# Kernel optimization log

Measured on AMD Instinct MI355X. Metric: run time of the kernel, lower is better.

## Reference

```python
import jax, jax.numpy as jnp
import numpy as np

H = 300          # node_hidden_dim (GINE output dim)
D = 2 * H        # set2set in_channels = 600
STEPS = 2        # num_step_set2_set


def _lstm_cell(x, h, c, W_ih, W_hh, b_ih, b_hh):
    # PyTorch LSTM gate order: i, f, g, o
    gates = x @ W_ih.T + h @ W_hh.T + b_ih + b_hh
    i, f, g, o = jnp.split(gates, 4, axis=-1)
    c = jax.nn.sigmoid(f) * c + jax.nn.sigmoid(i) * jnp.tanh(g)
    h = jax.nn.sigmoid(o) * jnp.tanh(c)
    return h, c


def _set2set(x, batch, num_graphs, W_ih, W_hh, b_ih, b_hh):
    # torch_geometric Set2Set with processing_steps=STEPS, 1-layer LSTM
    B = num_graphs
    q_star = jnp.zeros((B, 2 * D), x.dtype)
    h = jnp.zeros((B, D), x.dtype)
    c = jnp.zeros((B, D), x.dtype)
    for _ in range(STEPS):
        h, c = _lstm_cell(q_star, h, c, W_ih, W_hh, b_ih, b_hh)
        q = h                                   # [B, D]
        e = jnp.sum(x * q[batch], axis=-1)      # [N]
        emax = jax.ops.segment_max(e, batch, num_segments=B)
        a = jnp.exp(e - emax[batch])
        asum = jax.ops.segment_sum(a, batch, num_segments=B)
        a = a / (asum[batch] + 1e-16)           # segment softmax
        r = jax.ops.segment_sum(a[:, None] * x, batch, num_segments=B)
        q_star = jnp.concatenate([q, r], axis=-1)   # [B, 2D]
    return q_star


def _l2norm(x):
    return x / jnp.maximum(jnp.linalg.norm(x, axis=1, keepdims=True), 1e-12)


def setup_inputs() -> dict:
    key = jax.random.key(0)
    ks = jax.random.split(key, 8)
    Nu, Nv, B = 8192, 8192, 256
    solute_x = jax.random.normal(ks[0], (Nu, H), jnp.float32)
    solvent_x = jax.random.normal(ks[1], (Nv, H), jnp.float32)
    solute_batch = jnp.sort(jax.random.randint(ks[2], (Nu,), 0, B)).astype(jnp.int32)
    solvent_batch = jnp.sort(jax.random.randint(ks[3], (Nv,), 0, B)).astype(jnp.int32)
    lstm_W_ih = jax.random.normal(ks[4], (4 * D, 2 * D), jnp.float32) * 0.02
    lstm_W_hh = jax.random.normal(ks[5], (4 * D, D), jnp.float32) * 0.02
    lstm_b_ih = jnp.zeros((4 * D,), jnp.float32)
    lstm_b_hh = jnp.zeros((4 * D,), jnp.float32)
    pred_W = jax.random.normal(ks[6], (1, 8 * H), jnp.float32) * 0.02
    pred_b = jnp.zeros((1,), jnp.float32)
    return {
        "solute_x": solute_x, "solvent_x": solvent_x,
        "solute_batch": solute_batch, "solvent_batch": solvent_batch,
        "num_graphs": B,
        "lstm_W_ih": lstm_W_ih, "lstm_W_hh": lstm_W_hh,
        "lstm_b_ih": lstm_b_ih, "lstm_b_hh": lstm_b_hh,
        "pred_W": pred_W, "pred_b": pred_b,
    }


def reference(solute_x, solvent_x, solute_batch, solvent_batch, num_graphs,
              lstm_W_ih, lstm_W_hh, lstm_b_ih, lstm_b_hh, pred_W, pred_b):
    # F.normalize(dim=1)
    su = _l2norm(solute_x)    # [Nu, H]
    sv = _l2norm(solvent_x)   # [Nv, H]
    # len_map = solute_len.T @ solvent_len == same-pair membership mask
    mask = (solute_batch[:, None] == solvent_batch[None, :]).astype(su.dtype)
    interaction_map = (su @ sv.T) * mask          # [Nu, Nv]
    ret_interaction_map = interaction_map
    solvent_prime = interaction_map.T @ su        # [Nv, H]
    solute_prime = interaction_map @ sv           # [Nu, H]
    su2 = jnp.concatenate([su, solute_prime], axis=1)    # [Nu, 2H]
    sv2 = jnp.concatenate([sv, solvent_prime], axis=1)   # [Nv, 2H]
    su_s2s = _set2set(su2, solute_batch, num_graphs, lstm_W_ih, lstm_W_hh, lstm_b_ih, lstm_b_hh)
    sv_s2s = _set2set(sv2, solvent_batch, num_graphs, lstm_W_ih, lstm_W_hh, lstm_b_ih, lstm_b_hh)
    final = jnp.concatenate([su_s2s, sv_s2s], axis=1)    # [B, 8H]
    predictions = final @ pred_W.T + pred_b              # [B, 1]
    return predictions, ret_interaction_map
```

## Files before the change

kernel.cpp:

```cpp
#include <hip/hip_runtime.h>
#include <math.h>

#define HDIM 300
#define DDIM 600
#define NGR  256

typedef float vf4 __attribute__((ext_vector_type(4)));

__device__ __forceinline__ float wred_sum(float v){
  #pragma unroll
  for(int o=32;o;o>>=1) v += __shfl_xor(v,o,64);
  return v;
}
__device__ __forceinline__ float wred_max(float v){
  #pragma unroll
  for(int o=32;o;o>>=1) v = fmaxf(v,__shfl_xor(v,o,64));
  return v;
}
__device__ __forceinline__ float sigm(float x){ return 1.f/(1.f+expf(-x)); }

__global__ __launch_bounds__(256) void k_norm(const float* __restrict__ xu,
    const float* __restrict__ xv, float* __restrict__ su, float* __restrict__ sv,
    int Nu, int Nv){
  int wid = (blockIdx.x * 256 + threadIdx.x) >> 6;
  int lane = threadIdx.x & 63;
  if (wid >= Nu + Nv) return;
  const float* src; float* dst;
  if (wid < Nu){ src = xu + (size_t)wid*HDIM; dst = su + (size_t)wid*HDIM; }
  else         { src = xv + (size_t)(wid-Nu)*HDIM; dst = sv + (size_t)(wid-Nu)*HDIM; }
  float v[5]; float s = 0.f;
  #pragma unroll
  for(int c=0;c<5;c++){ int k = lane + 64*c; float x = (k<HDIM)? src[k] : 0.f; v[c]=x; s += x*x; }
  s = wred_sum(s);
  float inv = 1.f / fmaxf(sqrtf(s), 1e-12f);
  #pragma unroll
  for(int c=0;c<5;c++){ int k = lane + 64*c; if (k<HDIM) dst[k] = v[c]*inv; }
}

__global__ __launch_bounds__(640) void k_off_h1(const int* __restrict__ ub,
    const int* __restrict__ vb, int Nu, int Nv, int* __restrict__ uoff,
    int* __restrict__ voff, const float* __restrict__ b_ih,
    const float* __restrict__ b_hh, float* __restrict__ h1, float* __restrict__ c1){
  int t = threadIdx.x;
  if (t < NGR){
    int lo=0, hi=Nu;
    while(lo<hi){ int mid=(lo+hi)>>1; if (ub[mid] < t) lo=mid+1; else hi=mid; }
    uoff[t]=lo; if (t==0) uoff[NGR]=Nu;
  } else if (t < 2*NGR){
    int g=t-NGR; int lo=0, hi=Nv;
    while(lo<hi){ int mid=(lo+hi)>>1; if (vb[mid] < g) lo=mid+1; else hi=mid; }
    voff[g]=lo; if (g==0) voff[NGR]=Nv;
  }
  if (t < DDIM){
    float gi = b_ih[t]        + b_hh[t];
    float gg = b_ih[1200+t]   + b_hh[1200+t];
    float go = b_ih[1800+t]   + b_hh[1800+t];
    float c  = sigm(gi)*tanhf(gg);
    c1[t]=c; h1[t]=sigm(go)*tanhf(c);
  }
}

template<bool WRITE_MAP>
__global__ __launch_bounds__(256) void k_prime(const float* __restrict__ xa,
    const float* __restrict__ xb, const int* __restrict__ mybatch,
    const int* __restrict__ ooff, float* __restrict__ prime,
    float* __restrict__ eout, const float* __restrict__ h1,
    float* __restrict__ mapbase, int Nother){
  int i = blockIdx.x;
  int tid = threadIdx.x, lane = tid & 63, w = tid >> 6;
  __shared__ float xrow[HDIM];
  __shared__ float qv[2*HDIM];
  __shared__ float prl[4*304];
  __shared__ float red[4];
  const float* rowp = xa + (size_t)i*HDIM;
  for (int t=tid; t<HDIM;   t+=256) xrow[t] = rowp[t];
  for (int t=tid; t<2*HDIM; t+=256) qv[t]   = h1[t];
  int g = mybatch[i];
  int js = ooff[g], je = ooff[g+1];
  __syncthreads();
  if (WRITE_MAP){
    float* mrow = mapbase + (size_t)i*Nother;
    const vf4 z4 = {0.f,0.f,0.f,0.f};
    int nf4 = Nother >> 2;
    for (int q4=tid; q4<nf4; q4+=256){
      int j0 = q4*4;
      if (j0+4 <= js || j0 >= je){
        __builtin_nontemporal_store(z4, (vf4*)(mrow + j0));
      } else {
        #pragma unroll
        for(int u=0;u<4;u++){ int j=j0+u; if (j<js || j>=je) mrow[j]=0.f; }
      }
    }
  }
  float pr[5];
  #pragma unroll
  for(int c=0;c<5;c++) pr[c]=0.f;
  for (int j = js + w; j < je; j += 4){
    const float* orow = xb + (size_t)j*HDIM;
    float xv[5]; float d = 0.f;
    #pragma unroll
    for(int c=0;c<5;c++){
      int k = lane + 64*c; float x=0.f, a=0.f;
      if (k<HDIM){ x = orow[k]; a = xrow[k]; }
      xv[c]=x; d += a*x;
    }
    d = wred_sum(d);
    if (WRITE_MAP && lane==0) mapbase[(size_t)i*Nother + j] = d;
    #pragma unroll
    for(int c=0;c<5;c++) pr[c] += d * xv[c];
  }
  #pragma unroll
  for(int c=0;c<5;c++){ int k = lane + 64*c; if (k<HDIM) prl[w*304 + k] = pr[c]; }
  __syncthreads();
  float ep = 0.f;
  for (int t=tid; t<HDIM; t+=256){
    float s = prl[t] + prl[304+t] + prl[608+t] + prl[912+t];
    prime[(size_t)i*HDIM + t] = s;
    ep += xrow[t]*qv[t] + s*qv[HDIM+t];
  }
  ep = wred_sum(ep);
  if (lane==0) red[w] = ep;
  __syncthreads();
  if (tid==0) eout[i] = red[0]+red[1]+red[2]+red[3];
}

__global__ __launch_bounds__(256) void k_r1(const float* __restrict__ su,
    const float* __restrict__ sv, const float* __restrict__ spr,
    const float* __restrict__ svp, const float* __restrict__ e1u,
    const float* __restrict__ e1v, const int* __restrict__ uoff,
    const int* __restrict__ voff, float* __restrict__ r1){
  int bs = blockIdx.x; int set = bs >> 8; int g = bs & 255;
  const float* x  = set? sv  : su;
  const float* pr = set? svp : spr;
  const float* e  = set? e1v : e1u;
  const int* off  = set? voff: uoff;
  int tid = threadIdx.x, lane = tid & 63, w = tid >> 6;
  __shared__ float al[2048]; __shared__ float red[4]; __shared__ float shv;
  int ns = off[g], ne = off[g+1]; int n = ne - ns;
  float m = -INFINITY;
  for (int t=ns+tid; t<ne; t+=256) m = fmaxf(m, e[t]);
  m = wred_max(m);
  if (lane==0) red[w]=m;
  __syncthreads();
  if (tid==0) shv = fmaxf(fmaxf(red[0],red[1]),fmaxf(red[2],red[3]));
  __syncthreads();
  float emax = shv;
  float s = 0.f;
  for (int t=tid; t<n; t+=256){ float a = expf(e[ns+t]-emax); if (t<2048) al[t]=a; s += a; }
  s = wred_sum(s);
  __syncthreads();
  if (lane==0) red[w]=s;
  __syncthreads();
  if (tid==0) shv = red[0]+red[1]+red[2]+red[3];
  __syncthreads();
  float inv = 1.f/(shv + 1e-16f);
  float acc[3] = {0.f,0.f,0.f};
  for (int nn=0; nn<n; nn++){
    float a = (nn<2048)? al[nn] : expf(e[ns+nn]-emax);
    const float* xr = x  + (size_t)(ns+nn)*HDIM;
    const float* pp = pr + (size_t)(ns+nn)*HDIM;
    #pragma unroll
    for(int u=0;u<3;u++){ int c = tid + u*256; if (c<DDIM){
        float xv = (c<HDIM)? xr[c] : pp[c-HDIM]; acc[u] += a*xv; } }
  }
  #pragma unroll
  for(int u=0;u<3;u++){ int c = tid + u*256; if (c<DDIM) r1[(size_t)bs*DDIM + c] = acc[u]*inv; }
}

__global__ __launch_bounds__(256) void k_gbase(const float* __restrict__ h1,
    const float* __restrict__ Wih, const float* __restrict__ Whh,
    const float* __restrict__ b_ih, const float* __restrict__ b_hh,
    float* __restrict__ gbase){
  int n = blockIdx.x*4 + (threadIdx.x >> 6); int lane = threadIdx.x & 63;
  if (n >= 2400) return;
  const float* wi = Wih + (size_t)n*1200;
  const float* wh = Whh + (size_t)n*600;
  float s = 0.f;
  for (int k=lane; k<DDIM; k+=64) s += h1[k]*(wi[k] + wh[k]);
  s = wred_sum(s);
  if (lane==0) gbase[n] = s + b_ih[n] + b_hh[n];
}

__global__ __launch_bounds__(256) void k_gemm(const float* __restrict__ r1,
    const float* __restrict__ Wih, float* __restrict__ g2){
  __shared__ __align__(16) float Al[16*64];
  __shared__ __align__(16) float Bl[16*64];
  int tid = threadIdx.x;
  int n0 = blockIdx.x*64, gs0 = blockIdx.y*64;
  int tx = tid & 15, ty = tid >> 4;
  int lk = tid & 15, lr = tid >> 4;
  float acc[4][4] = {};
  for (int kt=0; kt<600; kt+=16){
    int k = kt + lk;
    #pragma unroll
    for (int u=0; u<4; u++){
      int gl = lr + u*16;
      Al[lk*64 + gl] = (k<600)? r1[(size_t)(gs0+gl)*DDIM + k] : 0.f;
      int n = n0 + gl;
      Bl[lk*64 + gl] = (k<600 && n<2400)? Wih[(size_t)n*1200 + 600 + k] : 0.f;
    }
    __syncthreads();
    #pragma unroll
    for (int kk=0; kk<16; kk++){
      float4 av = *(const float4*)&Al[kk*64 + ty*4];
      float4 bv = *(const float4*)&Bl[kk*64 + tx*4];
      float a[4]={av.x,av.y,av.z,av.w}, b[4]={bv.x,bv.y,bv.z,bv.w};
      #pragma unroll
      for(int mm=0;mm<4;mm++)
        #pragma unroll
        for(int nn=0;nn<4;nn++) acc[mm][nn] += a[mm]*b[nn];
    }
    __syncthreads();
  }
  #pragma unroll
  for (int mm=0; mm<4; mm++){
    int gs = gs0 + ty*4 + mm;
    int n  = n0 + tx*4;
    if (n+4 <= 2400){
      float4 o = make_float4(acc[mm][0],acc[mm][1],acc[mm][2],acc[mm][3]);
      *(float4*)&g2[(size_t)gs*2400 + n] = o;
    } else {
      #pragma unroll
      for(int nn=0;nn<4;nn++) if (n+nn<2400) g2[(size_t)gs*2400 + n+nn] = acc[mm][nn];
    }
  }
}

__global__ __launch_bounds__(256) void k_lstm2(const float* __restrict__ g2,
    const float* __restrict__ gbase, const float* __restrict__ c1,
    float* __restrict__ h2){
  int idx = blockIdx.x*256 + threadIdx.x;
  if (idx >= 512*DDIM) return;
  int gs = idx / DDIM, d = idx - gs*DDIM;
  const float* gg = g2 + (size_t)gs*2400;
  float gi = gg[d]        + gbase[d];
  float gf = gg[600+d]    + gbase[600+d];
  float gG = gg[1200+d]   + gbase[1200+d];
  float go = gg[1800+d]   + gbase[1800+d];
  float c  = sigm(gf)*c1[d] + sigm(gi)*tanhf(gG);
  h2[idx] = sigm(go)*tanhf(c);
}

__global__ __launch_bounds__(256) void k_r2(const float* __restrict__ su,
    const float* __restrict__ sv, const float* __restrict__ spr,
    const float* __restrict__ svp, const int* __restrict__ uoff,
    const int* __restrict__ voff, const float* __restrict__ h2,
    const float* __restrict__ pW, float* __restrict__ e2u,
    float* __restrict__ e2v, float* __restrict__ ppart){
  int bs = blockIdx.x; int set = bs >> 8; int g = bs & 255;
  const float* x  = set? sv  : su;
  const float* pr = set? svp : spr;
  const int* off  = set? voff: uoff;
  float* e2       = set? e2v : e2u;
  int tid = threadIdx.x, lane = tid & 63, w = tid >> 6;
  __shared__ float q[DDIM]; __shared__ float al[2048];
  __shared__ float red[4]; __shared__ float shv;
  for (int t=tid; t<DDIM; t+=256) q[t] = h2[(size_t)bs*DDIM + t];
  int ns = off[g], ne = off[g+1]; int n = ne - ns;
  __syncthreads();
  for (int node = ns + w; node < ne; node += 4){
    const float* xr = x  + (size_t)node*HDIM;
    const float* pp = pr + (size_t)node*HDIM;
    float d = 0.f;
    #pragma unroll
    for(int c=0;c<10;c++){ int k = lane + 64*c; if (k<DDIM){
        float xv = (k<HDIM)? xr[k] : pp[k-HDIM]; d += xv*q[k]; } }
    d = wred_sum(d);
    if (lane==0) e2[node] = d;
  }
  __syncthreads();
  float m = -INFINITY;
  for (int t=ns+tid; t<ne; t+=256) m = fmaxf(m, e2[t]);
  m = wred_max(m);
  if (lane==0) red[w]=m;
  __syncthreads();
  if (tid==0) shv = fmaxf(fmaxf(red[0],red[1]),fmaxf(red[2],red[3]));
  __syncthreads();
  float emax = shv;
  float s = 0.f;
  for (int t=tid; t<n; t+=256){ float a = expf(e2[ns+t]-emax); if (t<2048) al[t]=a; s += a; }
  s = wred_sum(s);
  __syncthreads();
  if (lane==0) red[w]=s;
  __syncthreads();
  if (tid==0) shv = red[0]+red[1]+red[2]+red[3];
  __syncthreads();
  float inv = 1.f/(shv + 1e-16f);
  float acc[3] = {0.f,0.f,0.f};
  for (int nn=0; nn<n; nn++){
    float a = (nn<2048)? al[nn] : expf(e2[ns+nn]-emax);
    const float* xr = x  + (size_t)(ns+nn)*HDIM;
    const float* pp = pr + (size_t)(ns+nn)*HDIM;
    #pragma unroll
    for(int u=0;u<3;u++){ int c = tid + u*256; if (c<DDIM){
        float xv = (c<HDIM)? xr[c] : pp[c-HDIM]; acc[u] += a*xv; } }
  }
  int hoff = set? 1200 : 0;
  float p = 0.f;
  #pragma unroll
  for(int u=0;u<3;u++){ int c = tid + u*256; if (c<DDIM) p += (acc[u]*inv)*pW[hoff+600+c]; }
  for (int t=tid; t<DDIM; t+=256) p += q[t]*pW[hoff+t];
  p = wred_sum(p);
  __syncthreads();
  if (lane==0) red[w] = p;
  __syncthreads();
  if (tid==0) ppart[bs] = red[0]+red[1]+red[2]+red[3];
}

__global__ __launch_bounds__(256) void k_pred(const float* __restrict__ ppart,
    const float* __restrict__ pred_b, float* __restrict__ out){
  int g = threadIdx.x;
  out[g] = ppart[g] + ppart[NGR+g] + pred_b[0];
}

extern "C" void kernel_launch(void* const* d_in, const int* in_sizes, int n_in,
                              void* d_out, int out_size, void* d_ws, size_t ws_size,
                              hipStream_t stream) {
  const float* solute_x  = (const float*)d_in[0];
  const float* solvent_x = (const float*)d_in[1];
  const int*   ub        = (const int*)d_in[2];
  const int*   vb        = (const int*)d_in[3];
  const float* Wih  = (const float*)d_in[5];
  const float* Whh  = (const float*)d_in[6];
  const float* b_ih = (const float*)d_in[7];
  const float* b_hh = (const float*)d_in[8];
  const float* pW   = (const float*)d_in[9];
  const float* pb   = (const float*)d_in[10];

  int Nu = in_sizes[0] / HDIM;
  int Nv = in_sizes[1] / HDIM;

  float* out = (float*)d_out;
  int predn = out_size - Nu*Nv;
  float* mapbase = out + predn;

  float* ws = (float*)d_ws;
  float* su    = ws;
  float* sv    = su    + (size_t)Nu*HDIM;
  float* spr   = sv    + (size_t)Nv*HDIM;
  float* svp   = spr   + (size_t)Nu*HDIM;
  float* e1u   = svp   + (size_t)Nv*HDIM;
  float* e1v   = e1u   + Nu;
  float* h1    = e1v   + Nv;
  float* c1    = h1    + DDIM;
  float* r1    = c1    + DDIM;
  float* gbase = r1    + 512*DDIM;
  float* g2    = gbase + 2400;
  float* h2    = g2    + (size_t)512*2400;
  float* ppart = h2    + 512*DDIM;
  int*   uoff  = (int*)(ppart + 512);
  int*   voff  = uoff + 257;

  k_norm<<<dim3((Nu+Nv)/4), dim3(256), 0, stream>>>(solute_x, solvent_x, su, sv, Nu, Nv);
  k_off_h1<<<dim3(1), dim3(640), 0, stream>>>(ub, vb, Nu, Nv, uoff, voff, b_ih, b_hh, h1, c1);
  k_prime<true ><<<dim3(Nu), dim3(256), 0, stream>>>(su, sv, ub, voff, spr, e1u, h1, mapbase, Nv);
  k_prime<false><<<dim3(Nv), dim3(256), 0, stream>>>(sv, su, vb, uoff, svp, e1v, h1, nullptr, Nv);
  k_r1<<<dim3(512), dim3(256), 0, stream>>>(su, sv, spr, svp, e1u, e1v, uoff, voff, r1);
  k_gbase<<<dim3(600), dim3(256), 0, stream>>>(h1, Wih, Whh, b_ih, b_hh, gbase);
  k_gemm<<<dim3(38, 8), dim3(256), 0, stream>>>(r1, Wih, g2);
  k_lstm2<<<dim3((512*DDIM + 255)/256), dim3(256), 0, stream>>>(g2, gbase, c1, h2);
  k_r2<<<dim3(512), dim3(256), 0, stream>>>(su, sv, spr, svp, uoff, voff, h2, pW, e1u, e1v, ppart);
  k_pred<<<dim3(1), dim3(NGR), 0, stream>>>(ppart, pb, out);
}
```

Before: 590.9 us.

## Fuse kernels, vectorize row loads, and fold LSTM gating into gate GEMM

Merges ten launches into five. Normalization is combined with offset and h1 setup, the two prime passes become one grid, and the r1 and gbase kernels share a launch. The gate GEMM is re-tiled so each block holds all four gates for 16 hidden units, which lets it apply the LSTM cell in its epilogue and drops the g2 round trip through memory. Row loads move to float4 vectors, and the final prediction is accumulated with atomics into an output pre-seeded with the bias. The goal is to cut launch overhead and intermediate global traffic, at the cost of atomic ordering nondeterminism and heterogeneous block roles.

```diff
diff --git a/kernel.cpp b/kernel.cpp
--- a/kernel.cpp
+++ b/kernel.cpp
@@ -19,58 +19,70 @@
 }
 __device__ __forceinline__ float sigm(float x){ return 1.f/(1.f+expf(-x)); }
 
-__global__ __launch_bounds__(256) void k_norm(const float* __restrict__ xu,
+__global__ __launch_bounds__(256) void k_norm_off(const float* __restrict__ xu,
     const float* __restrict__ xv, float* __restrict__ su, float* __restrict__ sv,
-    int Nu, int Nv){
-  int wid = (blockIdx.x * 256 + threadIdx.x) >> 6;
+    int Nu, int Nv, const int* __restrict__ ub, const int* __restrict__ vb,
+    int* __restrict__ uoff, int* __restrict__ voff,
+    const float* __restrict__ b_ih, const float* __restrict__ b_hh,
+    float* __restrict__ h1, float* __restrict__ c1,
+    const float* __restrict__ pb, float* __restrict__ outp){
+  if (blockIdx.x == gridDim.x - 1){
+    int t = threadIdx.x;
+    if (t < NGR){
+      int lo=0, hi=Nu;
+      while(lo<hi){ int m=(lo+hi)>>1; if (ub[m] < t) lo=m+1; else hi=m; }
+      uoff[t]=lo;
+      lo=0; hi=Nv;
+      while(lo<hi){ int m=(lo+hi)>>1; if (vb[m] < t) lo=m+1; else hi=m; }
+      voff[t]=lo;
+      if (t==0){ uoff[NGR]=Nu; voff[NGR]=Nv; }
+      outp[t] = pb[0];
+    }
+    for (int d=threadIdx.x; d<DDIM; d+=256){
+      float gi = b_ih[d]      + b_hh[d];
+      float gg = b_ih[1200+d] + b_hh[1200+d];
+      float go = b_ih[1800+d] + b_hh[1800+d];
+      float c  = sigm(gi)*tanhf(gg);
+      c1[d]=c; h1[d]=sigm(go)*tanhf(c);
+    }
+    return;
+  }
+  int wid = blockIdx.x*4 + (threadIdx.x >> 6);
   int lane = threadIdx.x & 63;
-  if (wid >= Nu + Nv) return;
   const float* src; float* dst;
   if (wid < Nu){ src = xu + (size_t)wid*HDIM; dst = su + (size_t)wid*HDIM; }
   else         { src = xv + (size_t)(wid-Nu)*HDIM; dst = sv + (size_t)(wid-Nu)*HDIM; }
-  float v[5]; float s = 0.f;
-  #pragma unroll
-  for(int c=0;c<5;c++){ int k = lane + 64*c; float x = (k<HDIM)? src[k] : 0.f; v[c]=x; s += x*x; }
+  const vf4* s4 = (const vf4*)src;
+  vf4 A = s4[lane];
+  vf4 Bv = (lane<11)? s4[64+lane] : (vf4){0.f,0.f,0.f,0.f};
+  float s = A.x*A.x+A.y*A.y+A.z*A.z+A.w*A.w + Bv.x*Bv.x+Bv.y*Bv.y+Bv.z*Bv.z+Bv.w*Bv.w;
   s = wred_sum(s);
   float inv = 1.f / fmaxf(sqrtf(s), 1e-12f);
-  #pragma unroll
-  for(int c=0;c<5;c++){ int k = lane + 64*c; if (k<HDIM) dst[k] = v[c]*inv; }
-}
-
-__global__ __launch_bounds__(640) void k_off_h1(const int* __restrict__ ub,
-    const int* __restrict__ vb, int Nu, int Nv, int* __restrict__ uoff,
-    int* __restrict__ voff, const float* __restrict__ b_ih,
-    const float* __restrict__ b_hh, float* __restrict__ h1, float* __restrict__ c1){
-  int t = threadIdx.x;
-  if (t < NGR){
-    int lo=0, hi=Nu;
-    while(lo<hi){ int mid=(lo+hi)>>1; if (ub[mid] < t) lo=mid+1; else hi=mid; }
-    uoff[t]=lo; if (t==0) uoff[NGR]=Nu;
-  } else if (t < 2*NGR){
-    int g=t-NGR; int lo=0, hi=Nv;
-    while(lo<hi){ int mid=(lo+hi)>>1; if (vb[mid] < g) lo=mid+1; else hi=mid; }
-    voff[g]=lo; if (g==0) voff[NGR]=Nv;
-  }
-  if (t < DDIM){
-    float gi = b_ih[t]        + b_hh[t];
-    float gg = b_ih[1200+t]   + b_hh[1200+t];
-    float go = b_ih[1800+t]   + b_hh[1800+t];
-    float c  = sigm(gi)*tanhf(gg);
-    c1[t]=c; h1[t]=sigm(go)*tanhf(c);
-  }
-}
-
-template<bool WRITE_MAP>
-__global__ __launch_bounds__(256) void k_prime(const float* __restrict__ xa,
-    const float* __restrict__ xb, const int* __restrict__ mybatch,
-    const int* __restrict__ ooff, float* __restrict__ prime,
-    float* __restrict__ eout, const float* __restrict__ h1,
-    float* __restrict__ mapbase, int Nother){
-  int i = blockIdx.x;
+  vf4* d4 = (vf4*)dst;
+  d4[lane] = A*inv;
+  if (lane<11) d4[64+lane] = Bv*inv;
+}
+
+__global__ __launch_bounds__(256) void k_prime(const float* __restrict__ su,
+    const float* __restrict__ sv, const int* __restrict__ ub,
+    const int* __restrict__ vb, const int* __restrict__ uoff,
+    const int* __restrict__ voff, float* __restrict__ spr,
+    float* __restrict__ svp, float* __restrict__ e1u, float* __restrict__ e1v,
+    const float* __restrict__ h1, float* __restrict__ mapbase, int Nu, int Nv){
+  int b = blockIdx.x;
+  bool isU = (b < Nu);
+  int i = isU ? b : b - Nu;
+  const float* xa = isU ? su : sv;
+  const float* xb = isU ? sv : su;
+  const int* mybatch = isU ? ub : vb;
+  const int* ooff    = isU ? voff : uoff;
+  float* prime = isU ? spr : svp;
+  float* eout  = isU ? e1u : e1v;
+
   int tid = threadIdx.x, lane = tid & 63, w = tid >> 6;
-  __shared__ float xrow[HDIM];
+  __shared__ __align__(16) float xrow[304];
+  __shared__ __align__(16) float prl[4*304];
   __shared__ float qv[2*HDIM];
-  __shared__ float prl[4*304];
   __shared__ float red[4];
   const float* rowp = xa + (size_t)i*HDIM;
   for (int t=tid; t<HDIM;   t+=256) xrow[t] = rowp[t];
@@ -78,10 +90,11 @@
   int g = mybatch[i];
   int js = ooff[g], je = ooff[g+1];
   __syncthreads();
-  if (WRITE_MAP){
-    float* mrow = mapbase + (size_t)i*Nother;
+
+  if (isU){
+    float* mrow = mapbase + (size_t)i*Nv;
     const vf4 z4 = {0.f,0.f,0.f,0.f};
-    int nf4 = Nother >> 2;
+    int nf4 = Nv >> 2;
     for (int q4=tid; q4<nf4; q4+=256){
       int j0 = q4*4;
       if (j0+4 <= js || j0 >= je){
@@ -92,25 +105,25 @@
       }
     }
   }
-  float pr[5];
-  #pragma unroll
-  for(int c=0;c<5;c++) pr[c]=0.f;
+
+  const vf4* x4 = (const vf4*)xrow;
+  vf4 xA = x4[lane];
+  vf4 xB = (lane<11)? x4[64+lane] : (vf4){0.f,0.f,0.f,0.f};
+  vf4 prA = {0.f,0.f,0.f,0.f}, prB = {0.f,0.f,0.f,0.f};
   for (int j = js + w; j < je; j += 4){
-    const float* orow = xb + (size_t)j*HDIM;
-    float xv[5]; float d = 0.f;
-    #pragma unroll
-    for(int c=0;c<5;c++){
-      int k = lane + 64*c; float x=0.f, a=0.f;
-      if (k<HDIM){ x = orow[k]; a = xrow[k]; }
-      xv[c]=x; d += a*x;
-    }
+    const vf4* orow = (const vf4*)(xb + (size_t)j*HDIM);
+    vf4 oA = orow[lane];
+    vf4 oB = (lane<11)? orow[64+lane] : (vf4){0.f,0.f,0.f,0.f};
+    float d = oA.x*xA.x + oA.y*xA.y + oA.z*xA.z + oA.w*xA.w
+            + oB.x*xB.x + oB.y*xB.y + oB.z*xB.z + oB.w*xB.w;
     d = wred_sum(d);
-    if (WRITE_MAP && lane==0) mapbase[(size_t)i*Nother + j] = d;
-    #pragma unroll
-    for(int c=0;c<5;c++) pr[c] += d * xv[c];
-  }
-  #pragma unroll
-  for(int c=0;c<5;c++){ int k = lane + 64*c; if (k<HDIM) prl[w*304 + k] = pr[c]; }
+    if (isU && lane==0) mapbase[(size_t)i*Nv + j] = d;
+    prA += d * oA;
+    prB += d * oB;
+  }
+  vf4* p4 = (vf4*)(prl + w*304);
+  p4[lane] = prA;
+  if (lane<11) p4[64+lane] = prB;
   __syncthreads();
   float ep = 0.f;
   for (int t=tid; t<HDIM; t+=256){
@@ -124,17 +137,31 @@
   if (tid==0) eout[i] = red[0]+red[1]+red[2]+red[3];
 }
 
-__global__ __launch_bounds__(256) void k_r1(const float* __restrict__ su,
+__global__ __launch_bounds__(256) void k_r1_gbase(const float* __restrict__ su,
     const float* __restrict__ sv, const float* __restrict__ spr,
     const float* __restrict__ svp, const float* __restrict__ e1u,
     const float* __restrict__ e1v, const int* __restrict__ uoff,
-    const int* __restrict__ voff, float* __restrict__ r1){
+    const int* __restrict__ voff, float* __restrict__ r1,
+    const float* __restrict__ h1, const float* __restrict__ Wih,
+    const float* __restrict__ Whh, const float* __restrict__ b_ih,
+    const float* __restrict__ b_hh, float* __restrict__ gbase){
+  int tid = threadIdx.x, lane = tid & 63, w = tid >> 6;
+  if (blockIdx.x >= 512){
+    int n = (blockIdx.x - 512)*4 + w;
+    if (n >= 2400) return;
+    const float* wi = Wih + (size_t)n*1200;
+    const float* wh = Whh + (size_t)n*600;
+    float s = 0.f;
+    for (int k=lane; k<DDIM; k+=64) s += h1[k]*(wi[k] + wh[k]);
+    s = wred_sum(s);
+    if (lane==0) gbase[n] = s + b_ih[n] + b_hh[n];
+    return;
+  }
   int bs = blockIdx.x; int set = bs >> 8; int g = bs & 255;
   const float* x  = set? sv  : su;
   const float* pr = set? svp : spr;
   const float* e  = set? e1v : e1u;
   const int* off  = set? voff: uoff;
-  int tid = threadIdx.x, lane = tid & 63, w = tid >> 6;
   __shared__ float al[2048]; __shared__ float red[4]; __shared__ float shv;
   int ns = off[g], ne = off[g+1]; int n = ne - ns;
   float m = -INFINITY;
@@ -167,78 +194,66 @@
   for(int u=0;u<3;u++){ int c = tid + u*256; if (c<DDIM) r1[(size_t)bs*DDIM + c] = acc[u]*inv; }
 }
 
-__global__ __launch_bounds__(256) void k_gbase(const float* __restrict__ h1,
-    const float* __restrict__ Wih, const float* __restrict__ Whh,
-    const float* __restrict__ b_ih, const float* __restrict__ b_hh,
-    float* __restrict__ gbase){
-  int n = blockIdx.x*4 + (threadIdx.x >> 6); int lane = threadIdx.x & 63;
-  if (n >= 2400) return;
-  const float* wi = Wih + (size_t)n*1200;
-  const float* wh = Whh + (size_t)n*600;
-  float s = 0.f;
-  for (int k=lane; k<DDIM; k+=64) s += h1[k]*(wi[k] + wh[k]);
-  s = wred_sum(s);
-  if (lane==0) gbase[n] = s + b_ih[n] + b_hh[n];
-}
-
-__global__ __launch_bounds__(256) void k_gemm(const float* __restrict__ r1,
-    const float* __restrict__ Wih, float* __restrict__ g2){
-  __shared__ __align__(16) float Al[16*64];
-  __shared__ __align__(16) float Bl[16*64];
+__global__ __launch_bounds__(256) void k_gemm_lstm(const float* __restrict__ r1,
+    const float* __restrict__ Wih, const float* __restrict__ gbase,
+    const float* __restrict__ c1, float* __restrict__ h2){
+  __shared__ __align__(16) float smem[64*68];
+  float* Al = smem;
+  float* Bl = smem + 16*68;
   int tid = threadIdx.x;
-  int n0 = blockIdx.x*64, gs0 = blockIdx.y*64;
+  int d0  = blockIdx.x*16;
+  int gs0 = blockIdx.y*64;
   int tx = tid & 15, ty = tid >> 4;
   int lk = tid & 15, lr = tid >> 4;
   float acc[4][4] = {};
   for (int kt=0; kt<600; kt+=16){
     int k = kt + lk;
+    bool kok = (k < 600);
     #pragma unroll
     for (int u=0; u<4; u++){
-      int gl = lr + u*16;
-      Al[lk*64 + gl] = (k<600)? r1[(size_t)(gs0+gl)*DDIM + k] : 0.f;
-      int n = n0 + gl;
-      Bl[lk*64 + gl] = (k<600 && n<2400)? Wih[(size_t)n*1200 + 600 + k] : 0.f;
+      int rl = lr + u*16;
+      Al[lk*68 + rl] = kok ? r1[(size_t)(gs0+rl)*DDIM + k] : 0.f;
+      int gate = rl >> 4, dd = rl & 15;
+      int d = d0 + dd;
+      Bl[lk*68 + rl] = (kok && d < 600)
+          ? Wih[(size_t)(gate*600 + d)*1200 + 600 + k] : 0.f;
     }
     __syncthreads();
     #pragma unroll
     for (int kk=0; kk<16; kk++){
-      float4 av = *(const float4*)&Al[kk*64 + ty*4];
-      float4 bv = *(const float4*)&Bl[kk*64 + tx*4];
-      float a[4]={av.x,av.y,av.z,av.w}, b[4]={bv.x,bv.y,bv.z,bv.w};
+      vf4 av = ((const vf4*)(Al + kk*68))[ty];
+      vf4 bv = ((const vf4*)(Bl + kk*68))[tx];
+      float a[4]={av.x,av.y,av.z,av.w}, bb[4]={bv.x,bv.y,bv.z,bv.w};
       #pragma unroll
       for(int mm=0;mm<4;mm++)
         #pragma unroll
-        for(int nn=0;nn<4;nn++) acc[mm][nn] += a[mm]*b[nn];
+        for(int nn=0;nn<4;nn++) acc[mm][nn] += a[mm]*bb[nn];
     }
     __syncthreads();
   }
   #pragma unroll
   for (int mm=0; mm<4; mm++){
-    int gs = gs0 + ty*4 + mm;
-    int n  = n0 + tx*4;
-    if (n+4 <= 2400){
-      float4 o = make_float4(acc[mm][0],acc[mm][1],acc[mm][2],acc[mm][3]);
-      *(float4*)&g2[(size_t)gs*2400 + n] = o;
-    } else {
-      #pragma unroll
-      for(int nn=0;nn<4;nn++) if (n+nn<2400) g2[(size_t)gs*2400 + n+nn] = acc[mm][nn];
-    }
-  }
-}
-
-__global__ __launch_bounds__(256) void k_lstm2(const float* __restrict__ g2,
-    const float* __restrict__ gbase, const float* __restrict__ c1,
-    float* __restrict__ h2){
-  int idx = blockIdx.x*256 + threadIdx.x;
-  if (idx >= 512*DDIM) return;
-  int gs = idx / DDIM, d = idx - gs*DDIM;
-  const float* gg = g2 + (size_t)gs*2400;
-  float gi = gg[d]        + gbase[d];
-  float gf = gg[600+d]    + gbase[600+d];
-  float gG = gg[1200+d]   + gbase[1200+d];
-  float go = gg[1800+d]   + gbase[1800+d];
-  float c  = sigm(gf)*c1[d] + sigm(gi)*tanhf(gG);
-  h2[idx] = sigm(go)*tanhf(c);
+    vf4 o = {acc[mm][0], acc[mm][1], acc[mm][2], acc[mm][3]};
+    ((vf4*)(smem + (ty*4+mm)*68))[tx] = o;
+  }
+  __syncthreads();
+  int d_l = tid & 15, r0 = tid >> 4;
+  int d = d0 + d_l;
+  if (d < 600){
+    float gb_i = gbase[d], gb_f = gbase[600+d], gb_g = gbase[1200+d], gb_o = gbase[1800+d];
+    float cc1 = c1[d];
+    #pragma unroll
+    for (int u=0; u<4; u++){
+      int rl = r0 + u*16;
+      const float* gr = smem + rl*68;
+      float gi = gr[d_l]      + gb_i;
+      float gf = gr[16+d_l]   + gb_f;
+      float gG = gr[32+d_l]   + gb_g;
+      float go = gr[48+d_l]   + gb_o;
+      float c  = sigm(gf)*cc1 + sigm(gi)*tanhf(gG);
+      h2[(size_t)(gs0+rl)*DDIM + d] = sigm(go)*tanhf(c);
+    }
+  }
 }
 
 __global__ __launch_bounds__(256) void k_r2(const float* __restrict__ su,
@@ -246,7 +261,7 @@
     const float* __restrict__ svp, const int* __restrict__ uoff,
     const int* __restrict__ voff, const float* __restrict__ h2,
     const float* __restrict__ pW, float* __restrict__ e2u,
-    float* __restrict__ e2v, float* __restrict__ ppart){
+    float* __restrict__ e2v, float* __restrict__ outp){
   int bs = blockIdx.x; int set = bs >> 8; int g = bs & 255;
   const float* x  = set? sv  : su;
   const float* pr = set? svp : spr;
@@ -304,13 +319,7 @@
   __syncthreads();
   if (lane==0) red[w] = p;
   __syncthreads();
-  if (tid==0) ppart[bs] = red[0]+red[1]+red[2]+red[3];
-}
-
-__global__ __launch_bounds__(256) void k_pred(const float* __restrict__ ppart,
-    const float* __restrict__ pred_b, float* __restrict__ out){
-  int g = threadIdx.x;
-  out[g] = ppart[g] + ppart[NGR+g] + pred_b[0];
+  if (tid==0) atomicAdd(&outp[g], red[0]+red[1]+red[2]+red[3]);
 }
 
 extern "C" void kernel_launch(void* const* d_in, const int* in_sizes, int n_in,
@@ -345,20 +354,18 @@
   float* c1    = h1    + DDIM;
   float* r1    = c1    + DDIM;
   float* gbase = r1    + 512*DDIM;
-  float* g2    = gbase + 2400;
-  float* h2    = g2    + (size_t)512*2400;
-  float* ppart = h2    + 512*DDIM;
-  int*   uoff  = (int*)(ppart + 512);
+  float* h2    = gbase + 2400;
+  int*   uoff  = (int*)(h2 + 512*DDIM);
   int*   voff  = uoff + 257;
 
-  k_norm<<<dim3((Nu+Nv)/4), dim3(256), 0, stream>>>(solute_x, solvent_x, su, sv, Nu, Nv);
-  k_off_h1<<<dim3(1), dim3(640), 0, stream>>>(ub, vb, Nu, Nv, uoff, voff, b_ih, b_hh, h1, c1);
-  k_prime<true ><<<dim3(Nu), dim3(256), 0, stream>>>(su, sv, ub, voff, spr, e1u, h1, mapbase, Nv);
-  k_prime<false><<<dim3(Nv), dim3(256), 0, stream>>>(sv, su, vb, uoff, svp, e1v, h1, nullptr, Nv);
-  k_r1<<<dim3(512), dim3(256), 0, stream>>>(su, sv, spr, svp, e1u, e1v, uoff, voff, r1);
-  k_gbase<<<dim3(600), dim3(256), 0, stream>>>(h1, Wih, Whh, b_ih, b_hh, gbase);
-  k_gemm<<<dim3(38, 8), dim3(256), 0, stream>>>(r1, Wih, g2);
-  k_lstm2<<<dim3((512*DDIM + 255)/256), dim3(256), 0, stream>>>(g2, gbase, c1, h2);
-  k_r2<<<dim3(512), dim3(256), 0, stream>>>(su, sv, spr, svp, uoff, voff, h2, pW, e1u, e1v, ppart);
-  k_pred<<<dim3(1), dim3(NGR), 0, stream>>>(ppart, pb, out);
-}
+  k_norm_off<<<dim3((Nu+Nv)/4 + 1), dim3(256), 0, stream>>>(
+      solute_x, solvent_x, su, sv, Nu, Nv, ub, vb, uoff, voff,
+      b_ih, b_hh, h1, c1, pb, out);
+  k_prime<<<dim3(Nu+Nv), dim3(256), 0, stream>>>(
+      su, sv, ub, vb, uoff, voff, spr, svp, e1u, e1v, h1, mapbase, Nu, Nv);
+  k_r1_gbase<<<dim3(512+600), dim3(256), 0, stream>>>(
+      su, sv, spr, svp, e1u, e1v, uoff, voff, r1, h1, Wih, Whh, b_ih, b_hh, gbase);
+  k_gemm_lstm<<<dim3(38, 8), dim3(256), 0, stream>>>(r1, Wih, gbase, c1, h2);
+  k_r2<<<dim3(512), dim3(256), 0, stream>>>(
+      su, sv, spr, svp, uoff, voff, h2, pW, e1u, e1v, out);
+}
```

Measured after the change: 576.5 us. 1.03x faster.
